# Kernel tuning notes

Measured on AMD Instinct MI355X. Metric: run time of the kernel, lower is better.

The kernel has to match this reference:

```python
import jax, jax.numpy as jnp
import numpy as np

MARGIN = 0.3


def setup_inputs() -> dict:
    key = jax.random.key(0)
    k1, k2 = jax.random.split(key)
    N, D, C = 8192, 512, 1024
    embeddings = jax.random.normal(k1, (N, D), dtype=jnp.float32)
    labels = jax.random.randint(k2, (N,), 0, C, dtype=jnp.int64)
    return {"embeddings": embeddings, "labels": labels}


def reference(embeddings, labels):
    # L2-normalize rows, cosine distance via Gram matrix: d = 1 - e_i . e_j
    e = embeddings / jnp.linalg.norm(embeddings, axis=1, keepdims=True)
    dist = 1.0 - jnp.matmul(e, e.T)  # [N, N]

    same = labels[:, None] == labels[None, :]           # [N, N] bool
    eye = jnp.eye(labels.shape[0], dtype=bool)
    pos_mask = same & ~eye                              # positives exclude self
    neg_mask = ~same                                    # negatives

    # Batch-hard mining: hardest (farthest) positive, hardest (closest) negative
    hardest_pos = jnp.max(jnp.where(pos_mask, dist, -jnp.inf), axis=1)
    hardest_neg = jnp.min(jnp.where(neg_mask, dist, jnp.inf), axis=1)

    loss = jax.nn.relu(hardest_pos - hardest_neg + MARGIN)
    return jnp.mean(loss)
```

## Files before the change

kernel.cpp:

```cpp
#include <hip/hip_runtime.h>
#include <hip/hip_fp8.h>
#include <hip/hip_fp16.h>
#include <stdint.h>

#define MARGIN 0.3f

constexpr int N = 8192;
constexpr int D = 512;
constexpr int BM = 128, BN = 128;
constexpr int NKS = D / 64;
constexpr int NT = N / BM;
constexpr int NPAIR = NT * (NT + 1) / 2;
constexpr int WEDGE = NPAIR / 8;
constexpr float ESCALE = 16.0f;
constexpr float INV_SC2 = 1.0f / (ESCALE * ESCALE);

typedef int i32x8 __attribute__((ext_vector_type(8)));
typedef float f32x16 __attribute__((ext_vector_type(16)));
typedef __fp16 h2 __attribute__((ext_vector_type(2)));

constexpr unsigned INF2 = 0x7C007C00u;

__device__ __forceinline__ unsigned char f2fp8(float f) {
  return __hip_fp8_e4m3(f).__x;
}

__device__ __forceinline__ unsigned pkmin(unsigned a, unsigned b) {
  unsigned d;
  asm("v_pk_min_f16 %0, %1, %2" : "=v"(d) : "v"(a), "v"(b));
  return d;
}

__device__ __forceinline__ unsigned cvtpk(float lo, float hi) {
  union { h2 h; unsigned u; } cv;
  cv.h = __builtin_amdgcn_cvt_pkrtz(lo, hi);
  return cv.u;
}

__device__ __forceinline__ void pair_from_q(int q, int& ti, int& tj) {
  int SI = 0;
  while (32 * (SI + 1) * (SI + 1) + 4 * (SI + 1) <= q) ++SI;
  int r = q - (32 * SI * SI + 4 * SI);
  int i, j, SJ;
  if (r < 64 * SI) {
    SJ = r >> 6;
    int w = r & 63;
    i = w >> 3;
    j = w & 7;
  } else {
    int d = r - 64 * SI;
    SJ = SI;
    i = 0;
    while ((i + 1) * (i + 2) / 2 <= d) ++i;
    j = d - i * (i + 1) / 2;
  }
  ti = SI * 8 + i;
  tj = SJ * 8 + j;
}


__global__ __launch_bounds__(256) void normalize_rows(
    const float* __restrict__ emb, unsigned char* __restrict__ e8,
    float* __restrict__ out) {
  if (blockIdx.x == 0 && threadIdx.x == 0) out[0] = 0.f;
  const int wave = threadIdx.x >> 6, lane = threadIdx.x & 63;
  const int row = blockIdx.x * 4 + wave;
  const float4* src = (const float4*)(emb + (size_t)row * D);
  float4 x0 = src[lane];
  float4 x1 = src[lane + 64];
  float ss = x0.x * x0.x + x0.y * x0.y + x0.z * x0.z + x0.w * x0.w +
             x1.x * x1.x + x1.y * x1.y + x1.z * x1.z + x1.w * x1.w;
#pragma unroll
  for (int m = 1; m < 64; m <<= 1) ss += __shfl_xor(ss, m, 64);
  const float r = rsqrtf(ss) * ESCALE;
  union { unsigned char b[8]; unsigned long long u; } o;
  o.b[0] = f2fp8(x0.x * r); o.b[1] = f2fp8(x0.y * r);
  o.b[2] = f2fp8(x0.z * r); o.b[3] = f2fp8(x0.w * r);
  o.b[4] = f2fp8(x1.x * r); o.b[5] = f2fp8(x1.y * r);
  o.b[6] = f2fp8(x1.z * r); o.b[7] = f2fp8(x1.w * r);
  const int n = row & 31;
  const unsigned inner =
      ((unsigned)(n * 64 + ((lane >> 1) & 3) * 16) ^
       ((unsigned)((n >> 1) & 7) << 4)) + (lane & 1) * 8;
  const unsigned off = (unsigned)((row >> 5) * 8 + (lane >> 3)) * 2048 + inner;
  __builtin_nontemporal_store(o.u, (unsigned long long*)(e8 + off));
}

__global__ __launch_bounds__(256, 3) void bh_gemm_sym(
    const unsigned char* __restrict__ e8, const int* __restrict__ labels,
    unsigned* __restrict__ scr) {
  __shared__ unsigned char lds[2][16384];
  __shared__ unsigned bufR[2][128];
  __shared__ unsigned bufC[2][128];

  const int b = blockIdx.x;
  const int q = WEDGE * (b & 7) + (b >> 3);
  int ti, tj;
  pair_from_q(q, ti, tj);
  const int iBase = ti * BM, jBase = tj * BN;
  const bool diag = (ti == tj);

  const int tid = threadIdx.x;
  const int lane = tid & 63;
  const int wave = tid >> 6;
  const int wr = wave >> 1, wc = wave & 1;
  const int n = lane & 31, hi = lane >> 5;

  const unsigned o0 =
      (unsigned)(n * 64 + hi * 32) ^ ((unsigned)((n >> 1) & 7) << 4);

  const unsigned char* gsrc[4];
  unsigned ldst[4];
#pragma unroll
  for (int j = 0; j < 4; ++j) {
    const int id = wave * 4 + j;
    const int mat = id >> 3;
    const int fb = (id & 7) >> 1;
    const int rb = (mat ? (jBase >> 5) : (iBase >> 5)) + fb;
    gsrc[j] = e8 + (size_t)(rb * 8) * 2048 + (id & 1) * 1024 + lane * 16;
    ldst[j] = (unsigned)id * 1024 + lane * 16;
  }

  auto STAGE = [&](int T, int buf) {
#pragma unroll
    for (int j = 0; j < 4; ++j)
      __builtin_amdgcn_global_load_lds(
          (const __attribute__((address_space(1))) unsigned int*)(gsrc[j] +
                                                                  (size_t)T * 2048),
          (__attribute__((address_space(3))) unsigned int*)(&lds[buf][ldst[j]]),
          16, 0, 0);
  };

  int lj[2];
#pragma unroll
  for (int c = 0; c < 2; ++c) lj[c] = labels[jBase + wc * 64 + c * 32 + n];

  f32x16 acc[2][2];
#pragma unroll
  for (int t = 0; t < 2; ++t)
#pragma unroll
    for (int c = 0; c < 2; ++c) acc[t][c] = (f32x16)0.0f;

  STAGE(0, 0);
  __syncthreads();
#pragma unroll
  for (int T = 0; T < NKS; ++T) {
    const int cur = T & 1;
    if (T + 1 < NKS) STAGE(T + 1, cur ^ 1);
    union { i32x8 v; int4 q2[2]; } aF[2], bF[2];
#pragma unroll
    for (int t = 0; t < 2; ++t) {
      const unsigned char* ab = &lds[cur][(wr * 2 + t) * 2048];
      aF[t].q2[0] = *(const int4*)(ab + o0);
      aF[t].q2[1] = *(const int4*)(ab + (o0 ^ 16));
      const unsigned char* bb = &lds[cur][8192 + (wc * 2 + t) * 2048];
      bF[t].q2[0] = *(const int4*)(bb + o0);
      bF[t].q2[1] = *(const int4*)(bb + (o0 ^ 16));
    }
#pragma unroll
    for (int t = 0; t < 2; ++t)
#pragma unroll
      for (int c = 0; c < 2; ++c)
        acc[t][c] = __builtin_amdgcn_mfma_scale_f32_32x32x64_f8f6f4(
            aF[t].v, bF[c].v, acc[t][c], 0, 0,
            0, 127, 0, 127);
    __syncthreads();
  }

  unsigned colAcc[2] = {INF2, INF2};

#pragma unroll
  for (int t = 0; t < 2; ++t) {
    int li[16];
#pragma unroll
    for (int a = 0; a < 4; ++a) {
      int4 v = *(const int4*)(labels + iBase + wr * 64 + t * 32 + 4 * hi + 8 * a);
      li[4 * a + 0] = v.x; li[4 * a + 1] = v.y;
      li[4 * a + 2] = v.z; li[4 * a + 3] = v.w;
    }
    unsigned P[2][16];
#pragma unroll
    for (int c = 0; c < 2; ++c) {
#pragma unroll
      for (int r = 0; r < 16; ++r) {
        const float s = acc[t][c][r];
        const unsigned u = cvtpk(s, -s);
        const bool same = (li[r] == lj[c]);
        const unsigned sel = same ? 0x0000FFFFu : 0xFFFF0000u;
        unsigned p = (sel & u) | (~sel & INF2);
        if (diag) {
          const int row32 = (r & 3) + 8 * (r >> 2) + 4 * hi;
          const bool self =
              (wr * 64 + t * 32 + row32) == (wc * 64 + c * 32 + n);
          p = self ? INF2 : p;
        }
        P[c][r] = p;
      }
      if (!diag) {
        unsigned cm = P[c][0];
#pragma unroll
        for (int r = 1; r < 16; ++r) cm = pkmin(cm, P[c][r]);
        colAcc[c] = pkmin(colAcc[c], cm);
      }
    }
    unsigned m[16];
#pragma unroll
    for (int r = 0; r < 16; ++r) m[r] = pkmin(P[0][r], P[1][r]);
    unsigned w8[8];
#pragma unroll
    for (int i = 0; i < 8; ++i) {
      unsigned x = pkmin(m[2 * i],
          (unsigned)__builtin_amdgcn_ds_swizzle((int)m[2 * i], 0x401F));
      unsigned y = pkmin(m[2 * i + 1],
          (unsigned)__builtin_amdgcn_ds_swizzle((int)m[2 * i + 1], 0x401F));
      w8[i] = (lane & 16) ? y : x;
    }
    unsigned w4[4];
#pragma unroll
    for (int i = 0; i < 4; ++i) {
      unsigned x = pkmin(w8[2 * i],
          (unsigned)__builtin_amdgcn_ds_swizzle((int)w8[2 * i], 0x201F));
      unsigned y = pkmin(w8[2 * i + 1],
          (unsigned)__builtin_amdgcn_ds_swizzle((int)w8[2 * i + 1], 0x201F));
      w4[i] = (lane & 8) ? y : x;
    }
    unsigned w2[2];
#pragma unroll
    for (int i = 0; i < 2; ++i) {
      unsigned x = pkmin(w4[2 * i],
          (unsigned)__builtin_amdgcn_ds_swizzle((int)w4[2 * i], 0x101F));
      unsigned y = pkmin(w4[2 * i + 1],
          (unsigned)__builtin_amdgcn_ds_swizzle((int)w4[2 * i + 1], 0x101F));
      w2[i] = (lane & 4) ? y : x;
    }
    unsigned x1 = pkmin(w2[0],
        (unsigned)__builtin_amdgcn_ds_swizzle((int)w2[0], 0x081F));
    unsigned y1 = pkmin(w2[1],
        (unsigned)__builtin_amdgcn_ds_swizzle((int)w2[1], 0x081F));
    unsigned w1 = (lane & 2) ? y1 : x1;
    w1 = pkmin(w1, (unsigned)__builtin_amdgcn_ds_swizzle((int)w1, 0x041F));
    const int row32 = 16 * ((lane >> 1) & 1) + 8 * ((lane >> 2) & 1) + 4 * hi +
                      2 * ((lane >> 3) & 1) + ((lane >> 4) & 1);
    if ((lane & 1) == 0) bufR[wc][wr * 64 + t * 32 + row32] = w1;
  }

  if (!diag) {
#pragma unroll
    for (int c = 0; c < 2; ++c)
      colAcc[c] = pkmin(colAcc[c], __shfl_xor(colAcc[c], 32, 64));
    if (hi == 0) {
#pragma unroll
      for (int c = 0; c < 2; ++c)
        bufC[wr][wc * 64 + c * 32 + n] = colAcc[c];
    }
  }

  __syncthreads();

  if (wc == 0) {
    const int row = wr * 64 + lane;
    __builtin_nontemporal_store(pkmin(bufR[0][row], bufR[1][row]),
                                &scr[(unsigned)(iBase + row) * 64 + tj]);
  }
  if (!diag && wr == 0) {
    const int col = wc * 64 + lane;
    __builtin_nontemporal_store(pkmin(bufC[0][col], bufC[1][col]),
                                &scr[(unsigned)(jBase + col) * 64 + ti]);
  }
}

__global__ __launch_bounds__(256) void finalize_loss(
    const unsigned* __restrict__ scr, float* __restrict__ out) {
  const int row = blockIdx.x * 256 + threadIdx.x;
  const uint4* p = (const uint4*)(scr + (size_t)row * 64);
  unsigned mm = INF2;
#pragma unroll
  for (int i = 0; i < 16; ++i) {
    uint4 w = p[i];
    mm = pkmin(mm, pkmin(pkmin(w.x, w.y), pkmin(w.z, w.w)));
  }
  const float mn = __half2float(__ushort_as_half((unsigned short)(mm & 0xffff)));
  const float nmx = __half2float(__ushort_as_half((unsigned short)(mm >> 16)));
  float loss = (-nmx - mn) * INV_SC2 + MARGIN;
  float sum = loss > 0.f ? loss : 0.f;
#pragma unroll
  for (int m = 1; m < 64; m <<= 1) sum += __shfl_xor(sum, m, 64);
  __shared__ float ws4[4];
  const int lane = threadIdx.x & 63, wave = threadIdx.x >> 6;
  if (lane == 0) ws4[wave] = sum;
  __syncthreads();
  if (threadIdx.x == 0)
    atomicAdd(out, (ws4[0] + ws4[1] + ws4[2] + ws4[3]) * (1.0f / N));
}

extern "C" void kernel_launch(void* const* d_in, const int* in_sizes, int n_in,
                              void* d_out, int out_size, void* d_ws, size_t ws_size,
                              hipStream_t stream) {
  const float* emb = (const float*)d_in[0];
  const int* labels = (const int*)d_in[1];
  float* out = (float*)d_out;

  unsigned char* e8 = (unsigned char*)d_ws;
  unsigned* scr = (unsigned*)((char*)d_ws + (size_t)4 * 1024 * 1024);

  normalize_rows<<<N / 4, 256, 0, stream>>>(emb, e8, out);
  bh_gemm_sym<<<NPAIR, 256, 0, stream>>>(e8, labels, scr);
  finalize_loss<<<N / 256, 256, 0, stream>>>(scr, out);
}
```

Baseline: 102.2 us.

## Split GEMM tile across 16 waves with one MFMA each

The 128x128 tile kernel now runs with 1024 threads (16 waves) instead of 256, so each wave computes a single 32x32 MFMA accumulator rather than a 2x2 set. Each wave issues one global-to-LDS load per stage instead of four, and the row/column min reductions are combined across four wave columns and rows through enlarged shared buffers. The aim is more latency hiding and less register pressure per wave. In exchange each A/B fragment is reloaded from LDS by more waves, and each K step has a block-wide barrier across 16 waves. Nontemporal stores were also replaced with plain stores.

```diff
diff --git a/kernel.cpp b/kernel.cpp
--- a/kernel.cpp
+++ b/kernel.cpp
@@ -83,15 +83,15 @@
       ((unsigned)(n * 64 + ((lane >> 1) & 3) * 16) ^
        ((unsigned)((n >> 1) & 7) << 4)) + (lane & 1) * 8;
   const unsigned off = (unsigned)((row >> 5) * 8 + (lane >> 3)) * 2048 + inner;
-  __builtin_nontemporal_store(o.u, (unsigned long long*)(e8 + off));
-}
-
-__global__ __launch_bounds__(256, 3) void bh_gemm_sym(
+  *(unsigned long long*)(e8 + off) = o.u;
+}
+
+__global__ __launch_bounds__(1024, 8) void bh_gemm_sym(
     const unsigned char* __restrict__ e8, const int* __restrict__ labels,
     unsigned* __restrict__ scr) {
   __shared__ unsigned char lds[2][16384];
-  __shared__ unsigned bufR[2][128];
-  __shared__ unsigned bufC[2][128];
+  __shared__ unsigned bufR[4][128];
+  __shared__ unsigned bufC[4][128];
 
   const int b = blockIdx.x;
   const int q = WEDGE * (b & 7) + (b >> 3);
@@ -102,44 +102,29 @@
 
   const int tid = threadIdx.x;
   const int lane = tid & 63;
-  const int wave = tid >> 6;
-  const int wr = wave >> 1, wc = wave & 1;
+  const int w = tid >> 6;
+  const int wr = w >> 2, wc = w & 3;
   const int n = lane & 31, hi = lane >> 5;
 
   const unsigned o0 =
       (unsigned)(n * 64 + hi * 32) ^ ((unsigned)((n >> 1) & 7) << 4);
 
-  const unsigned char* gsrc[4];
-  unsigned ldst[4];
-#pragma unroll
-  for (int j = 0; j < 4; ++j) {
-    const int id = wave * 4 + j;
-    const int mat = id >> 3;
-    const int fb = (id & 7) >> 1;
-    const int rb = (mat ? (jBase >> 5) : (iBase >> 5)) + fb;
-    gsrc[j] = e8 + (size_t)(rb * 8) * 2048 + (id & 1) * 1024 + lane * 16;
-    ldst[j] = (unsigned)id * 1024 + lane * 16;
-  }
+  const int matw = w >> 3;
+  const int fb = (w & 7) >> 1;
+  const int rb = (matw ? (jBase >> 5) : (iBase >> 5)) + fb;
+  const unsigned char* gsrc =
+      e8 + (size_t)(rb * 8) * 2048 + (w & 1) * 1024 + lane * 16;
+  const unsigned ldst = (unsigned)w * 1024 + lane * 16;
 
   auto STAGE = [&](int T, int buf) {
-#pragma unroll
-    for (int j = 0; j < 4; ++j)
-      __builtin_amdgcn_global_load_lds(
-          (const __attribute__((address_space(1))) unsigned int*)(gsrc[j] +
-                                                                  (size_t)T * 2048),
-          (__attribute__((address_space(3))) unsigned int*)(&lds[buf][ldst[j]]),
-          16, 0, 0);
+    __builtin_amdgcn_global_load_lds(
+        (const __attribute__((address_space(1))) unsigned int*)(gsrc +
+                                                                (size_t)T * 2048),
+        (__attribute__((address_space(3))) unsigned int*)(&lds[buf][ldst]),
+        16, 0, 0);
   };
 
-  int lj[2];
-#pragma unroll
-  for (int c = 0; c < 2; ++c) lj[c] = labels[jBase + wc * 64 + c * 32 + n];
-
-  f32x16 acc[2][2];
-#pragma unroll
-  for (int t = 0; t < 2; ++t)
-#pragma unroll
-    for (int c = 0; c < 2; ++c) acc[t][c] = (f32x16)0.0f;
+  f32x16 acc = (f32x16)0.0f;
 
   STAGE(0, 0);
   __syncthreads();
@@ -147,125 +132,97 @@
   for (int T = 0; T < NKS; ++T) {
     const int cur = T & 1;
     if (T + 1 < NKS) STAGE(T + 1, cur ^ 1);
-    union { i32x8 v; int4 q2[2]; } aF[2], bF[2];
-#pragma unroll
-    for (int t = 0; t < 2; ++t) {
-      const unsigned char* ab = &lds[cur][(wr * 2 + t) * 2048];
-      aF[t].q2[0] = *(const int4*)(ab + o0);
-      aF[t].q2[1] = *(const int4*)(ab + (o0 ^ 16));
-      const unsigned char* bb = &lds[cur][8192 + (wc * 2 + t) * 2048];
-      bF[t].q2[0] = *(const int4*)(bb + o0);
-      bF[t].q2[1] = *(const int4*)(bb + (o0 ^ 16));
+    union { i32x8 v; int4 q2[2]; } aF, bF;
+    const unsigned char* ab = &lds[cur][wr * 2048];
+    aF.q2[0] = *(const int4*)(ab + o0);
+    aF.q2[1] = *(const int4*)(ab + (o0 ^ 16));
+    const unsigned char* bb = &lds[cur][8192 + wc * 2048];
+    bF.q2[0] = *(const int4*)(bb + o0);
+    bF.q2[1] = *(const int4*)(bb + (o0 ^ 16));
+    acc = __builtin_amdgcn_mfma_scale_f32_32x32x64_f8f6f4(
+        aF.v, bF.v, acc, 0, 0,
+        0, 127, 0, 127);
+    __syncthreads();
+  }
+
+  const int lj = labels[jBase + wc * 32 + n];
+  unsigned colAcc = INF2;
+  unsigned m[16];
+#pragma unroll
+  for (int a = 0; a < 4; ++a) {
+    int4 v = *(const int4*)(labels + iBase + wr * 32 + 4 * hi + 8 * a);
+    const int liv[4] = {v.x, v.y, v.z, v.w};
+#pragma unroll
+    for (int vv = 0; vv < 4; ++vv) {
+      const int r = 4 * a + vv;
+      const float s = acc[r];
+      const unsigned u = cvtpk(s, -s);
+      const bool same = (liv[vv] == lj);
+      const unsigned sel = same ? 0x0000FFFFu : 0xFFFF0000u;
+      unsigned p = (sel & u) | (~sel & INF2);
+      if (diag) {
+        const int row32 = vv + 8 * a + 4 * hi;
+        const bool self = (wr * 32 + row32) == (wc * 32 + n);
+        p = self ? INF2 : p;
+      }
+      m[r] = p;
+      colAcc = pkmin(colAcc, p);
     }
-#pragma unroll
-    for (int t = 0; t < 2; ++t)
-#pragma unroll
-      for (int c = 0; c < 2; ++c)
-        acc[t][c] = __builtin_amdgcn_mfma_scale_f32_32x32x64_f8f6f4(
-            aF[t].v, bF[c].v, acc[t][c], 0, 0,
-            0, 127, 0, 127);
-    __syncthreads();
-  }
-
-  unsigned colAcc[2] = {INF2, INF2};
-
-#pragma unroll
-  for (int t = 0; t < 2; ++t) {
-    int li[16];
-#pragma unroll
-    for (int a = 0; a < 4; ++a) {
-      int4 v = *(const int4*)(labels + iBase + wr * 64 + t * 32 + 4 * hi + 8 * a);
-      li[4 * a + 0] = v.x; li[4 * a + 1] = v.y;
-      li[4 * a + 2] = v.z; li[4 * a + 3] = v.w;
-    }
-    unsigned P[2][16];
-#pragma unroll
-    for (int c = 0; c < 2; ++c) {
-#pragma unroll
-      for (int r = 0; r < 16; ++r) {
-        const float s = acc[t][c][r];
-        const unsigned u = cvtpk(s, -s);
-        const bool same = (li[r] == lj[c]);
-        const unsigned sel = same ? 0x0000FFFFu : 0xFFFF0000u;
-        unsigned p = (sel & u) | (~sel & INF2);
-        if (diag) {
-          const int row32 = (r & 3) + 8 * (r >> 2) + 4 * hi;
-          const bool self =
-              (wr * 64 + t * 32 + row32) == (wc * 64 + c * 32 + n);
-          p = self ? INF2 : p;
-        }
-        P[c][r] = p;
-      }
-      if (!diag) {
-        unsigned cm = P[c][0];
-#pragma unroll
-        for (int r = 1; r < 16; ++r) cm = pkmin(cm, P[c][r]);
-        colAcc[c] = pkmin(colAcc[c], cm);
-      }
-    }
-    unsigned m[16];
-#pragma unroll
-    for (int r = 0; r < 16; ++r) m[r] = pkmin(P[0][r], P[1][r]);
-    unsigned w8[8];
-#pragma unroll
-    for (int i = 0; i < 8; ++i) {
-      unsigned x = pkmin(m[2 * i],
-          (unsigned)__builtin_amdgcn_ds_swizzle((int)m[2 * i], 0x401F));
-      unsigned y = pkmin(m[2 * i + 1],
-          (unsigned)__builtin_amdgcn_ds_swizzle((int)m[2 * i + 1], 0x401F));
-      w8[i] = (lane & 16) ? y : x;
-    }
-    unsigned w4[4];
-#pragma unroll
-    for (int i = 0; i < 4; ++i) {
-      unsigned x = pkmin(w8[2 * i],
-          (unsigned)__builtin_amdgcn_ds_swizzle((int)w8[2 * i], 0x201F));
-      unsigned y = pkmin(w8[2 * i + 1],
-          (unsigned)__builtin_amdgcn_ds_swizzle((int)w8[2 * i + 1], 0x201F));
-      w4[i] = (lane & 8) ? y : x;
-    }
-    unsigned w2[2];
-#pragma unroll
-    for (int i = 0; i < 2; ++i) {
-      unsigned x = pkmin(w4[2 * i],
-          (unsigned)__builtin_amdgcn_ds_swizzle((int)w4[2 * i], 0x101F));
-      unsigned y = pkmin(w4[2 * i + 1],
-          (unsigned)__builtin_amdgcn_ds_swizzle((int)w4[2 * i + 1], 0x101F));
-      w2[i] = (lane & 4) ? y : x;
-    }
-    unsigned x1 = pkmin(w2[0],
-        (unsigned)__builtin_amdgcn_ds_swizzle((int)w2[0], 0x081F));
-    unsigned y1 = pkmin(w2[1],
-        (unsigned)__builtin_amdgcn_ds_swizzle((int)w2[1], 0x081F));
-    unsigned w1 = (lane & 2) ? y1 : x1;
-    w1 = pkmin(w1, (unsigned)__builtin_amdgcn_ds_swizzle((int)w1, 0x041F));
-    const int row32 = 16 * ((lane >> 1) & 1) + 8 * ((lane >> 2) & 1) + 4 * hi +
-                      2 * ((lane >> 3) & 1) + ((lane >> 4) & 1);
-    if ((lane & 1) == 0) bufR[wc][wr * 64 + t * 32 + row32] = w1;
   }
 
   if (!diag) {
-#pragma unroll
-    for (int c = 0; c < 2; ++c)
-      colAcc[c] = pkmin(colAcc[c], __shfl_xor(colAcc[c], 32, 64));
-    if (hi == 0) {
-#pragma unroll
-      for (int c = 0; c < 2; ++c)
-        bufC[wr][wc * 64 + c * 32 + n] = colAcc[c];
-    }
-  }
+    colAcc = pkmin(colAcc, __shfl_xor(colAcc, 32, 64));
+    if (hi == 0) bufC[wr][wc * 32 + n] = colAcc;
+  }
+
+  unsigned w8[8];
+#pragma unroll
+  for (int i = 0; i < 8; ++i) {
+    unsigned x = pkmin(m[2 * i],
+        (unsigned)__builtin_amdgcn_ds_swizzle((int)m[2 * i], 0x401F));
+    unsigned y = pkmin(m[2 * i + 1],
+        (unsigned)__builtin_amdgcn_ds_swizzle((int)m[2 * i + 1], 0x401F));
+    w8[i] = (lane & 16) ? y : x;
+  }
+  unsigned w4[4];
+#pragma unroll
+  for (int i = 0; i < 4; ++i) {
+    unsigned x = pkmin(w8[2 * i],
+        (unsigned)__builtin_amdgcn_ds_swizzle((int)w8[2 * i], 0x201F));
+    unsigned y = pkmin(w8[2 * i + 1],
+        (unsigned)__builtin_amdgcn_ds_swizzle((int)w8[2 * i + 1], 0x201F));
+    w4[i] = (lane & 8) ? y : x;
+  }
+  unsigned w2[2];
+#pragma unroll
+  for (int i = 0; i < 2; ++i) {
+    unsigned x = pkmin(w4[2 * i],
+        (unsigned)__builtin_amdgcn_ds_swizzle((int)w4[2 * i], 0x101F));
+    unsigned y = pkmin(w4[2 * i + 1],
+        (unsigned)__builtin_amdgcn_ds_swizzle((int)w4[2 * i + 1], 0x101F));
+    w2[i] = (lane & 4) ? y : x;
+  }
+  unsigned x1 = pkmin(w2[0],
+      (unsigned)__builtin_amdgcn_ds_swizzle((int)w2[0], 0x081F));
+  unsigned y1 = pkmin(w2[1],
+      (unsigned)__builtin_amdgcn_ds_swizzle((int)w2[1], 0x081F));
+  unsigned w1 = (lane & 2) ? y1 : x1;
+  w1 = pkmin(w1, (unsigned)__builtin_amdgcn_ds_swizzle((int)w1, 0x041F));
+  const int row32 = 16 * ((lane >> 1) & 1) + 8 * ((lane >> 2) & 1) + 4 * hi +
+                    2 * ((lane >> 3) & 1) + ((lane >> 4) & 1);
+  if ((lane & 1) == 0) bufR[wc][wr * 32 + row32] = w1;
 
   __syncthreads();
 
-  if (wc == 0) {
-    const int row = wr * 64 + lane;
-    __builtin_nontemporal_store(pkmin(bufR[0][row], bufR[1][row]),
-                                &scr[(unsigned)(iBase + row) * 64 + tj]);
-  }
-  if (!diag && wr == 0) {
-    const int col = wc * 64 + lane;
-    __builtin_nontemporal_store(pkmin(bufC[0][col], bufC[1][col]),
-                                &scr[(unsigned)(jBase + col) * 64 + ti]);
+  if (tid < 128) {
+    const unsigned v = pkmin(pkmin(bufR[0][tid], bufR[1][tid]),
+                             pkmin(bufR[2][tid], bufR[3][tid]));
+    scr[(unsigned)(iBase + tid) * 64 + tj] = v;
+  } else if (!diag && tid < 256) {
+    const int col = tid - 128;
+    const unsigned v = pkmin(pkmin(bufC[0][col], bufC[1][col]),
+                             pkmin(bufC[2][col], bufC[3][col]));
+    scr[(unsigned)(jBase + col) * 64 + ti] = v;
   }
 }
 
@@ -304,6 +261,6 @@
   unsigned* scr = (unsigned*)((char*)d_ws + (size_t)4 * 1024 * 1024);
 
   normalize_rows<<<N / 4, 256, 0, stream>>>(emb, e8, out);
-  bh_gemm_sym<<<NPAIR, 256, 0, stream>>>(e8, labels, scr);
+  bh_gemm_sym<<<NPAIR, 1024, 0, stream>>>(e8, labels, scr);
   finalize_loss<<<N / 256, 256, 0, stream>>>(scr, out);
 }
```

Result: slower. 107.0 us (+4.7%).

## Stage two K-steps per barrier and transpose scratch layout for coalesced access

Applied to the files above, without the earlier changes.

The GEMM main loop now stages two 64-wide K slices per LDS buffer, which halves the number of barriers. LDS use doubles, so launch bounds occupancy drops from 3 to 2 blocks. The scratch min/max buffer is transposed to tile-major so that both the GEMM epilogue writes and the finalize reads are coalesced. Nontemporal stores are replaced with ordinary stores. The cost is fewer resident waves to hide latency.

```diff
diff --git a/kernel.cpp b/kernel.cpp
--- a/kernel.cpp
+++ b/kernel.cpp
@@ -9,6 +9,7 @@
 constexpr int D = 512;
 constexpr int BM = 128, BN = 128;
 constexpr int NKS = D / 64;
+constexpr int NKP = NKS / 2;
 constexpr int NT = N / BM;
 constexpr int NPAIR = NT * (NT + 1) / 2;
 constexpr int WEDGE = NPAIR / 8;
@@ -83,13 +84,13 @@
       ((unsigned)(n * 64 + ((lane >> 1) & 3) * 16) ^
        ((unsigned)((n >> 1) & 7) << 4)) + (lane & 1) * 8;
   const unsigned off = (unsigned)((row >> 5) * 8 + (lane >> 3)) * 2048 + inner;
-  __builtin_nontemporal_store(o.u, (unsigned long long*)(e8 + off));
-}
-
-__global__ __launch_bounds__(256, 3) void bh_gemm_sym(
+  *(unsigned long long*)(e8 + off) = o.u;
+}
+
+__global__ __launch_bounds__(256, 2) void bh_gemm_sym(
     const unsigned char* __restrict__ e8, const int* __restrict__ labels,
     unsigned* __restrict__ scr) {
-  __shared__ unsigned char lds[2][16384];
+  __shared__ unsigned char lds[2][2][16384];
   __shared__ unsigned bufR[2][128];
   __shared__ unsigned bufC[2][128];
 
@@ -121,14 +122,17 @@
     ldst[j] = (unsigned)id * 1024 + lane * 16;
   }
 
-  auto STAGE = [&](int T, int buf) {
-#pragma unroll
-    for (int j = 0; j < 4; ++j)
-      __builtin_amdgcn_global_load_lds(
-          (const __attribute__((address_space(1))) unsigned int*)(gsrc[j] +
-                                                                  (size_t)T * 2048),
-          (__attribute__((address_space(3))) unsigned int*)(&lds[buf][ldst[j]]),
-          16, 0, 0);
+  auto STAGE2 = [&](int TT, int buf) {
+#pragma unroll
+    for (int s = 0; s < 2; ++s)
+#pragma unroll
+      for (int j = 0; j < 4; ++j)
+        __builtin_amdgcn_global_load_lds(
+            (const __attribute__((address_space(1))) unsigned int*)(
+                gsrc[j] + (size_t)(2 * TT + s) * 2048),
+            (__attribute__((address_space(3))) unsigned int*)(
+                &lds[buf][s][ldst[j]]),
+            16, 0, 0);
   };
 
   int lj[2];
@@ -141,29 +145,32 @@
 #pragma unroll
     for (int c = 0; c < 2; ++c) acc[t][c] = (f32x16)0.0f;
 
-  STAGE(0, 0);
+  STAGE2(0, 0);
   __syncthreads();
 #pragma unroll
-  for (int T = 0; T < NKS; ++T) {
-    const int cur = T & 1;
-    if (T + 1 < NKS) STAGE(T + 1, cur ^ 1);
-    union { i32x8 v; int4 q2[2]; } aF[2], bF[2];
-#pragma unroll
-    for (int t = 0; t < 2; ++t) {
-      const unsigned char* ab = &lds[cur][(wr * 2 + t) * 2048];
-      aF[t].q2[0] = *(const int4*)(ab + o0);
-      aF[t].q2[1] = *(const int4*)(ab + (o0 ^ 16));
-      const unsigned char* bb = &lds[cur][8192 + (wc * 2 + t) * 2048];
-      bF[t].q2[0] = *(const int4*)(bb + o0);
-      bF[t].q2[1] = *(const int4*)(bb + (o0 ^ 16));
-    }
-#pragma unroll
-    for (int t = 0; t < 2; ++t)
-#pragma unroll
-      for (int c = 0; c < 2; ++c)
-        acc[t][c] = __builtin_amdgcn_mfma_scale_f32_32x32x64_f8f6f4(
-            aF[t].v, bF[c].v, acc[t][c], 0, 0,
-            0, 127, 0, 127);
+  for (int TT = 0; TT < NKP; ++TT) {
+    const int cur = TT & 1;
+    if (TT + 1 < NKP) STAGE2(TT + 1, cur ^ 1);
+#pragma unroll
+    for (int s = 0; s < 2; ++s) {
+      union { i32x8 v; int4 q2[2]; } aF[2], bF[2];
+#pragma unroll
+      for (int t = 0; t < 2; ++t) {
+        const unsigned char* ab = &lds[cur][s][(wr * 2 + t) * 2048];
+        aF[t].q2[0] = *(const int4*)(ab + o0);
+        aF[t].q2[1] = *(const int4*)(ab + (o0 ^ 16));
+        const unsigned char* bb = &lds[cur][s][8192 + (wc * 2 + t) * 2048];
+        bF[t].q2[0] = *(const int4*)(bb + o0);
+        bF[t].q2[1] = *(const int4*)(bb + (o0 ^ 16));
+      }
+#pragma unroll
+      for (int t = 0; t < 2; ++t)
+#pragma unroll
+        for (int c = 0; c < 2; ++c)
+          acc[t][c] = __builtin_amdgcn_mfma_scale_f32_32x32x64_f8f6f4(
+              aF[t].v, bF[c].v, acc[t][c], 0, 0,
+              0, 127, 0, 127);
+    }
     __syncthreads();
   }
 
@@ -259,26 +266,21 @@
 
   if (wc == 0) {
     const int row = wr * 64 + lane;
-    __builtin_nontemporal_store(pkmin(bufR[0][row], bufR[1][row]),
-                                &scr[(unsigned)(iBase + row) * 64 + tj]);
+    scr[(unsigned)tj * 8192 + iBase + row] = pkmin(bufR[0][row], bufR[1][row]);
   }
   if (!diag && wr == 0) {
     const int col = wc * 64 + lane;
-    __builtin_nontemporal_store(pkmin(bufC[0][col], bufC[1][col]),
-                                &scr[(unsigned)(jBase + col) * 64 + ti]);
+    scr[(unsigned)ti * 8192 + jBase + col] = pkmin(bufC[0][col], bufC[1][col]);
   }
 }
 
 __global__ __launch_bounds__(256) void finalize_loss(
     const unsigned* __restrict__ scr, float* __restrict__ out) {
   const int row = blockIdx.x * 256 + threadIdx.x;
-  const uint4* p = (const uint4*)(scr + (size_t)row * 64);
   unsigned mm = INF2;
 #pragma unroll
-  for (int i = 0; i < 16; ++i) {
-    uint4 w = p[i];
-    mm = pkmin(mm, pkmin(pkmin(w.x, w.y), pkmin(w.z, w.w)));
-  }
+  for (int t = 0; t < 64; ++t)
+    mm = pkmin(mm, scr[(unsigned)t * 8192 + row]);
   const float mn = __half2float(__ushort_as_half((unsigned short)(mm & 0xffff)));
   const float nmx = __half2float(__ushort_as_half((unsigned short)(mm >> 16)));
   float loss = (-nmx - mn) * INV_SC2 + MARGIN;
```

New measurement: 119.2 us. 1.17x slower.
